# Performance work log

Hardware: AMD Instinct MI355X
Metric: run time of the kernel (lower is better)

## Reference

```python
import jax, jax.numpy as jnp
import numpy as np

D_MODEL = 1024
NUM_HEADS = 16
HEAD_DIM = D_MODEL // NUM_HEADS
THETA = 10000.0
B, T = 2, 2048


def setup_inputs() -> dict:
    key = jax.random.key(0)
    k1, k2, k3 = jax.random.split(key, 3)
    x = jax.random.normal(k1, (B, T, D_MODEL), dtype=jnp.float32)
    W_qkv = jax.random.normal(k2, (3 * D_MODEL, D_MODEL), dtype=jnp.float32) * 0.02
    W_o = jax.random.normal(k3, (D_MODEL, D_MODEL), dtype=jnp.float32) * 0.02
    return {"x": x, "W_qkv": W_qkv, "W_o": W_o}


def _rope(x, cos, sin):
    # x: [B, h, T, d]; rotate interleaved even/odd pairs
    x_even = x[..., 0::2]
    x_odd = x[..., 1::2]
    out_even = x_even * cos - x_odd * sin
    out_odd = x_even * sin + x_odd * cos
    out = jnp.stack([out_even, out_odd], axis=-1)  # [B,h,T,d/2,2]
    return out.reshape(x.shape)


def reference(x, W_qkv, W_o):
    b, t, dm = x.shape
    # fused QKV projection (bias-free Linear: x @ W.T)
    qkv = jnp.einsum('btd,ed->bte', x, W_qkv)                # [B,T,3*D]
    qkv = qkv.reshape(b, t, 3, NUM_HEADS, HEAD_DIM)
    qkv = jnp.transpose(qkv, (2, 0, 3, 1, 4))                # [3,B,h,T,d]
    q, k, v = qkv[0], qkv[1], qkv[2]

    # RoPE with token_positions = arange(T)
    pos = jnp.arange(t, dtype=jnp.float32)                   # [T]
    inv_freq = THETA ** (-jnp.arange(0, HEAD_DIM, 2, dtype=jnp.float32) / HEAD_DIM)
    ang = pos[:, None] * inv_freq[None, :]                   # [T, d/2]
    cos = jnp.cos(ang)[None, None, :, :]
    sin = jnp.sin(ang)[None, None, :, :]
    q = _rope(q, cos, sin)
    k = _rope(k, cos, sin)

    # causal scaled dot-product attention
    scale = 1.0 / jnp.sqrt(jnp.asarray(HEAD_DIM, dtype=x.dtype))
    scores = jnp.einsum('bhqd,bhkd->bhqk', q, k) * scale     # [B,h,T,T]
    causal = jnp.tril(jnp.ones((t, t), dtype=bool))
    scores = jnp.where(causal[None, None, :, :], scores, -jnp.inf)
    attn = jax.nn.softmax(scores, axis=-1)
    out = jnp.einsum('bhqk,bhkd->bhqd', attn, v)             # [B,h,T,d]
    out = jnp.transpose(out, (0, 2, 1, 3)).reshape(b, t, dm) # [B,T,D]
    return jnp.einsum('btd,ed->bte', out, W_o)
```

## Files before the change

kernel.cpp:

```cpp
#include <hip/hip_runtime.h>
#include <hip/hip_bf16.h>
#include <cstdint>

#define NHEADS 16
#define HDIM 64
#define BB 2
#define TSEQ 2048
#define DM 1024
#define MROWS (BB*TSEQ)

typedef unsigned short u16;
typedef unsigned int u32;
typedef __bf16 bf16x8 __attribute__((ext_vector_type(8)));
typedef float f32x4 __attribute__((ext_vector_type(4)));

#define AS1C(p) ((const __attribute__((address_space(1))) u32*)(p))
#define AS3(p)  ((__attribute__((address_space(3))) u32*)(p))

static __device__ __forceinline__ u16 f2bf(float f) {
  return __builtin_bit_cast(u16, __float2bfloat16(f));
}
static __device__ __forceinline__ float bf2f(u16 u) {
  return __bfloat162float(__builtin_bit_cast(__hip_bfloat16, u));
}
static __device__ __forceinline__ u32 pack2bf(float a, float b) {
  const u32 ua = __builtin_bit_cast(u32, a) + 0x8000u;
  const u32 ub = __builtin_bit_cast(u32, b) + 0x8000u;
  return (ua >> 16) | (ub & 0xFFFF0000u);
}
static __device__ __forceinline__ f32x4 mfma16x16(bf16x8 a, bf16x8 b, f32x4 c) {
  return __builtin_amdgcn_mfma_f32_16x16x32_bf16(a, b, c, 0, 0, 0);
}

#define N4_X   (MROWS * DM / 4)
#define N4_WQ  (3 * DM * DM / 4)
#define N4_WO  (DM * DM / 4)
__global__ __launch_bounds__(256) void cast_all(const float* __restrict__ x,
                                                const float* __restrict__ wq,
                                                const float* __restrict__ wo,
                                                u16* __restrict__ xb,
                                                u16* __restrict__ wqb,
                                                u16* __restrict__ wob) {
  int i = blockIdx.x * 256 + threadIdx.x;
  const int stride = gridDim.x * 256;
  for (; i < N4_X + N4_WQ + N4_WO; i += stride) {
    const float4* src; u16* dst; int j;
    if (i < N4_X)            { src = (const float4*)x;  dst = xb;  j = i; }
    else if (i < N4_X + N4_WQ) { src = (const float4*)wq; dst = wqb; j = i - N4_X; }
    else                     { src = (const float4*)wo; dst = wob; j = i - N4_X - N4_WQ; }
    float4 v = src[j];
    ushort4 o;
    o.x = f2bf(v.x); o.y = f2bf(v.y); o.z = f2bf(v.z); o.w = f2bf(v.w);
    ((ushort4*)dst)[j] = o;
  }
}

template<int WRITE_BF16>
__global__ __launch_bounds__(256, 2) void gemm_bt(const u16* __restrict__ A,
                                                  const u16* __restrict__ Bm,
                                                  float* __restrict__ Cf,
                                                  u16* __restrict__ Cb,
                                                  int M, int N, int K) {
  __shared__ u16 lA[2][128 * 32];
  __shared__ u16 lB[2][128 * 32];
  const int tid = threadIdx.x;
  const int w = tid >> 6, l = tid & 63;
  const int wr = w >> 1, wc = w & 1;
  int bid = blockIdx.y * gridDim.x + blockIdx.x;
  const int cpx = (gridDim.x * gridDim.y) >> 3;
  bid = (bid & 7) * cpx + (bid >> 3);
  const int bx = bid % gridDim.x, by = bid / gridDim.x;
  const int brow = by * 128, bcol = bx * 128;
  const int lr = l & 15, lg = l >> 4;

  const int srow = l >> 2;
  const int scol = (((l & 3) ^ (srow & 3)) * 8);

  auto stage = [&](int buf, int k0) {
#pragma unroll
    for (int is = 0; is < 2; ++is) {
      const int chunk = w * 2 + is;
      const int row = chunk * 16 + srow;
      __builtin_amdgcn_global_load_lds(AS1C(A + (size_t)(brow + row) * K + k0 + scol),
                                       AS3((char*)lA[buf] + chunk * 1024), 16, 0, 0);
      __builtin_amdgcn_global_load_lds(AS1C(Bm + (size_t)(bcol + row) * K + k0 + scol),
                                       AS3((char*)lB[buf] + chunk * 1024), 16, 0, 0);
    }
  };

  f32x4 acc[4][4] = {};
  const int nk = K >> 5;
  stage(0, 0);
  for (int kk = 0; kk < nk; ++kk) {
    const int cur = kk & 1;
    __syncthreads();
    if (kk + 1 < nk) stage(cur ^ 1, (kk + 1) << 5);
    bf16x8 af[4], bfr[4];
#pragma unroll
    for (int m = 0; m < 4; ++m) {
      const int row = wr * 64 + m * 16 + lr;
      const int sl = lg ^ (row & 3);
      af[m] = *(const bf16x8*)(&lA[cur][row * 32 + sl * 8]);
    }
#pragma unroll
    for (int n = 0; n < 4; ++n) {
      const int row = wc * 64 + n * 16 + lr;
      const int sl = lg ^ (row & 3);
      bfr[n] = *(const bf16x8*)(&lB[cur][row * 32 + sl * 8]);
    }
#pragma unroll
    for (int m = 0; m < 4; ++m)
#pragma unroll
      for (int n = 0; n < 4; ++n)
        acc[m][n] = mfma16x16(af[m], bfr[n], acc[m][n]);
  }
#pragma unroll
  for (int m = 0; m < 4; ++m)
#pragma unroll
    for (int n = 0; n < 4; ++n)
#pragma unroll
      for (int r = 0; r < 4; ++r) {
        const int row = brow + wr * 64 + m * 16 + lg * 4 + r;
        const int col = bcol + wc * 64 + n * 16 + lr;
        if constexpr (WRITE_BF16)
          Cb[(size_t)row * N + col] = f2bf(acc[m][n][r]);
        else
          Cf[(size_t)row * N + col] = acc[m][n][r];
      }
}

__global__ __launch_bounds__(256) void rope_reshape(const u16* __restrict__ qkvb,
                                                    u16* __restrict__ qb,
                                                    u16* __restrict__ kb,
                                                    u16* __restrict__ vbT) {
  const int bh = blockIdx.y;
  const int b = bh >> 4, h = bh & 15;
  const int t0 = blockIdx.x * 64;
  const int tid = threadIdx.x;
  const float C = -0.4152410118609203f;
  const float QS = 0.125f * 1.44269504088896341f;

  for (int idx = tid; idx < 64 * 32; idx += 256) {
    const int tl = idx >> 5, p = idx & 31;
    const int t = t0 + tl;
    const size_t base = ((size_t)(b * TSEQ + t)) * 3072 + h * 64 + 2 * p;
    const float qe = bf2f(qkvb[base]), qo = bf2f(qkvb[base + 1]);
    const float ke = bf2f(qkvb[base + 1024]), ko = bf2f(qkvb[base + 1025]);
    const float inv = exp2f((float)p * C);
    const float ang = (float)t * inv;
    float sn, cs;
    sincosf(ang, &sn, &cs);
    const size_t ob = ((size_t)bh * TSEQ + t) * 64 + 2 * p;
    qb[ob]     = f2bf((qe * cs - qo * sn) * QS);
    qb[ob + 1] = f2bf((qe * sn + qo * cs) * QS);
    kb[ob]     = f2bf(ke * cs - ko * sn);
    kb[ob + 1] = f2bf(ke * sn + ko * cs);
  }

  __shared__ u16 lT[64][65];
  for (int idx = tid; idx < 64 * 64; idx += 256) {
    const int tl = idx >> 6, d = idx & 63;
    lT[tl][d] = qkvb[((size_t)(b * TSEQ + t0 + tl)) * 3072 + 2048 + h * 64 + d];
  }
  __syncthreads();
  for (int idx = tid; idx < 64 * 64; idx += 256) {
    const int d = idx >> 6, tl = idx & 63;
    vbT[((size_t)bh * 64 + d) * TSEQ + t0 + tl] = lT[tl][d];
  }
}

__global__ __launch_bounds__(256, 4) void attn_fwd(const u16* __restrict__ qb,
                                                   const u16* __restrict__ kb,
                                                   const u16* __restrict__ vbT,
                                                   u16* __restrict__ ob) {
  __shared__ u16 lK[2][2][32 * 64];
  __shared__ u16 lV[2][2][64 * 32];
  __shared__ u16 lP[4][16 * 40];
  const int hw = blockIdx.x;
  const int logical = (hw & 7) * 64 + (hw >> 3);
  const int bh = logical >> 4;
  const int pair = logical & 15;
  const int b = bh >> 4, h = bh & 15;
  const int tid = threadIdx.x;
  const int w = tid >> 6, l = tid & 63;
  const int g = w >> 1, wq = w & 1;
  const int lr = l & 15, lg = l >> 4;
  const int kscol = ((l & 7) ^ (l >> 3)) * 8;
  const int vscol = ((l & 3) ^ ((l >> 2) & 3)) * 8;
  const u16* Kb = kb + (size_t)bh * TSEQ * 64;
  const u16* Vb = vbT + (size_t)bh * 64 * TSEQ;
  u16* lPw = lP[w];

  auto stage = [&](int buf, int kt) {
#pragma unroll
    for (int is = 0; is < 2; ++is) {
      const int chunk = wq * 2 + is;
      const int krow = chunk * 8 + (l >> 3);
      __builtin_amdgcn_global_load_lds(AS1C(Kb + (size_t)(kt * 32 + krow) * 64 + kscol),
                                       AS3((char*)lK[g][buf] + chunk * 1024), 16, 0, 0);
      const int vrow = chunk * 16 + (l >> 2);
      __builtin_amdgcn_global_load_lds(AS1C(Vb + (size_t)vrow * TSEQ + kt * 32 + vscol),
                                       AS3((char*)lV[g][buf] + chunk * 1024), 16, 0, 0);
    }
  };

  for (int half = 0; half < 2; ++half) {
    const int qt = half ? (31 - pair) : pair;
    const int q0 = qt * 64;
    const int ts = 2 * qt + wq;
    const int qa0 = q0 + wq * 32 + lr;

    bf16x8 qf[2][2];
    {
      const u16* qp = qb + ((size_t)bh * TSEQ + q0 + wq * 32 + lr) * 64 + lg * 8;
      qf[0][0] = *(const bf16x8*)qp;
      qf[0][1] = *(const bf16x8*)(qp + 32);
      qp += 16 * 64;
      qf[1][0] = *(const bf16x8*)qp;
      qf[1][1] = *(const bf16x8*)(qp + 32);
    }

    f32x4 o0[4] = {}, o1[4] = {};
    float ls0 = 0.f, ls1 = 0.f;

    __syncthreads();
    stage(0, g);
    for (int it = 0; it <= qt; ++it) {
      const int cur = it & 1;
      __syncthreads();
      if (it < qt) stage(cur ^ 1, 2 * (it + 1) + g);
      const int kt = 2 * it + g;
      if (kt <= ts) {
        const u16* Kc = lK[g][cur];
        const u16* Vc = lV[g][cur];

        bf16x8 kf[2][2];
#pragma unroll
        for (int n = 0; n < 2; ++n) {
          const int row = n * 16 + lr;
#pragma unroll
          for (int ks = 0; ks < 2; ++ks)
            kf[n][ks] = *(const bf16x8*)(&Kc[row * 64 + (((ks * 4 + lg) ^ (row & 7)) * 8)]);
        }
        f32x4 s0[2] = {}, s1[2] = {};
        __builtin_amdgcn_s_setprio(1);
#pragma unroll
        for (int n = 0; n < 2; ++n)
#pragma unroll
          for (int ks = 0; ks < 2; ++ks) {
            s0[n] = mfma16x16(kf[n][ks], qf[0][ks], s0[n]);
            s1[n] = mfma16x16(kf[n][ks], qf[1][ks], s1[n]);
          }
        __builtin_amdgcn_s_setprio(0);

        const bool diag = (kt == ts);
        const int kvb = kt * 32;

#pragma unroll
        for (int n = 0; n < 2; ++n) {
          float pv[4];
#pragma unroll
          for (int r = 0; r < 4; ++r) {
            float p = __builtin_amdgcn_exp2f(s0[n][r]);
            if (diag && (kvb + n * 16 + lg * 4 + r > qa0)) p = 0.f;
            pv[r] = p;
            ls0 += p;
          }
          uint2 pk; pk.x = pack2bf(pv[0], pv[1]); pk.y = pack2bf(pv[2], pv[3]);
          *(uint2*)(&lPw[lr * 40 + n * 16 + lg * 4]) = pk;
        }
        bf16x8 pf0 = *(const bf16x8*)(&lPw[lr * 40 + lg * 8]);

#pragma unroll
        for (int n = 0; n < 2; ++n) {
          float pv[4];
#pragma unroll
          for (int r = 0; r < 4; ++r) {
            float p = __builtin_amdgcn_exp2f(s1[n][r]);
            if (diag && (kvb + n * 16 + lg * 4 + r > qa0 + 16)) p = 0.f;
            pv[r] = p;
            ls1 += p;
          }
          uint2 pk; pk.x = pack2bf(pv[0], pv[1]); pk.y = pack2bf(pv[2], pv[3]);
          *(uint2*)(&lPw[lr * 40 + n * 16 + lg * 4]) = pk;
        }
        bf16x8 pf1 = *(const bf16x8*)(&lPw[lr * 40 + lg * 8]);

        __builtin_amdgcn_s_setprio(1);
#pragma unroll
        for (int n = 0; n < 4; ++n) {
          const int row = n * 16 + lr;
          bf16x8 vf = *(const bf16x8*)(&Vc[row * 32 + ((lg ^ (row & 3)) * 8)]);
          o0[n] = mfma16x16(vf, pf0, o0[n]);
          o1[n] = mfma16x16(vf, pf1, o1[n]);
        }
        __builtin_amdgcn_s_setprio(0);
      }
    }

    ls0 += __shfl_xor(ls0, 16); ls0 += __shfl_xor(ls0, 32);
    ls1 += __shfl_xor(ls1, 16); ls1 += __shfl_xor(ls1, 32);

    __syncthreads();
    float* mO = (float*)&lK[0][0][0];
    float* mL = (float*)&lV[0][0][0];
    if (g == 1) {
#pragma unroll
      for (int qs = 0; qs < 2; ++qs)
#pragma unroll
        for (int n = 0; n < 4; ++n)
#pragma unroll
          for (int r = 0; r < 4; ++r) {
            const int d = n * 16 + lg * 4 + r;
            mO[((wq * 2 + qs) * 64 + d) * 16 + lr] = (qs ? o1[n][r] : o0[n][r]);
          }
      if (lg == 0) {
        mL[(wq * 2 + 0) * 16 + lr] = ls0;
        mL[(wq * 2 + 1) * 16 + lr] = ls1;
      }
    }
    __syncthreads();
    if (g == 0) {
      const float rl0 = 1.f / (ls0 + mL[(wq * 2 + 0) * 16 + lr]);
      const float rl1 = 1.f / (ls1 + mL[(wq * 2 + 1) * 16 + lr]);
#pragma unroll
      for (int qs = 0; qs < 2; ++qs) {
        const int q = q0 + wq * 32 + qs * 16 + lr;
        const float rl = qs ? rl1 : rl0;
#pragma unroll
        for (int n = 0; n < 4; ++n) {
          ushort4 ov;
#pragma unroll
          for (int r = 0; r < 4; ++r) {
            const int d = n * 16 + lg * 4 + r;
            const float o = (qs ? o1[n][r] : o0[n][r]) + mO[((wq * 2 + qs) * 64 + d) * 16 + lr];
            ((u16*)&ov)[r] = f2bf(o * rl);
          }
          *(ushort4*)(&ob[(size_t)(b * TSEQ + q) * DM + h * 64 + n * 16 + lg * 4]) = ov;
        }
      }
    }
  }
}

extern "C" void kernel_launch(void* const* d_in, const int* in_sizes, int n_in,
                              void* d_out, int out_size, void* d_ws, size_t ws_size,
                              hipStream_t stream) {
  const float* x    = (const float*)d_in[0];
  const float* Wqkv = (const float*)d_in[1];
  const float* Wo   = (const float*)d_in[2];
  float* out = (float*)d_out;

  char* ws = (char*)d_ws;
  u16* xb    = (u16*)ws; ws += (size_t)MROWS * DM * 2;
  u16* wqkvb = (u16*)ws; ws += (size_t)3 * DM * DM * 2;
  u16* wob   = (u16*)ws; ws += (size_t)DM * DM * 2;
  u16* qkvb  = (u16*)ws; ws += (size_t)MROWS * 3 * DM * 2;
  u16* qb    = (u16*)ws; ws += (size_t)BB * NHEADS * TSEQ * HDIM * 2;
  u16* kb    = (u16*)ws; ws += (size_t)BB * NHEADS * TSEQ * HDIM * 2;
  u16* vbT   = (u16*)ws; ws += (size_t)BB * NHEADS * TSEQ * HDIM * 2;
  u16* ob    = (u16*)ws; ws += (size_t)MROWS * DM * 2;

  cast_all<<<2048, 256, 0, stream>>>(x, Wqkv, Wo, xb, wqkvb, wob);

  gemm_bt<1><<<dim3(3 * DM / 128, MROWS / 128), 256, 0, stream>>>(
      xb, wqkvb, nullptr, qkvb, MROWS, 3 * DM, DM);

  rope_reshape<<<dim3(TSEQ / 64, BB * NHEADS), 256, 0, stream>>>(qkvb, qb, kb, vbT);

  attn_fwd<<<512, 256, 0, stream>>>(qb, kb, vbT, ob);

  gemm_bt<0><<<dim3(DM / 128, MROWS / 128), 256, 0, stream>>>(
      ob, wob, out, nullptr, MROWS, DM, DM);
}
```

Before: 121.3 us.

## Split attention KV range into four partial blocks with a separate merge kernel

Each attention block now handles a 128-row query tile and one quarter of its causal KV range, giving 1024 blocks with all four waves working on separate query rows and sharing a single K/V stage. Partial unnormalized outputs (bf16) and row sums go to scratch that reuses the dead cast/QKV workspace. A new merge kernel sums them and normalizes. RoPE is also vectorized with 16-byte loads and stores and uses hardware sin/cos on a range-reduced angle. The intent is better load balance and occupancy, paid for with extra scratch traffic, an additional launch, and bf16 rounding of the partial sums.

```diff
diff --git a/kernel.cpp b/kernel.cpp
--- a/kernel.cpp
+++ b/kernel.cpp
@@ -139,22 +139,32 @@
   const int tid = threadIdx.x;
   const float C = -0.4152410118609203f;
   const float QS = 0.125f * 1.44269504088896341f;
-
-  for (int idx = tid; idx < 64 * 32; idx += 256) {
-    const int tl = idx >> 5, p = idx & 31;
+  const float R2PI = 0.15915494309189535f;
+
+  for (int idx = tid; idx < 64 * 8; idx += 256) {
+    const int tl = idx >> 3, grp = idx & 7;
     const int t = t0 + tl;
-    const size_t base = ((size_t)(b * TSEQ + t)) * 3072 + h * 64 + 2 * p;
-    const float qe = bf2f(qkvb[base]), qo = bf2f(qkvb[base + 1]);
-    const float ke = bf2f(qkvb[base + 1024]), ko = bf2f(qkvb[base + 1025]);
-    const float inv = exp2f((float)p * C);
-    const float ang = (float)t * inv;
-    float sn, cs;
-    sincosf(ang, &sn, &cs);
-    const size_t ob = ((size_t)bh * TSEQ + t) * 64 + 2 * p;
-    qb[ob]     = f2bf((qe * cs - qo * sn) * QS);
-    qb[ob + 1] = f2bf((qe * sn + qo * cs) * QS);
-    kb[ob]     = f2bf(ke * cs - ko * sn);
-    kb[ob + 1] = f2bf(ke * sn + ko * cs);
+    const size_t base = ((size_t)(b * TSEQ + t)) * 3072 + h * 64 + grp * 8;
+    u16 qv[8], kv8[8], qo[8], ko[8];
+    *(uint4*)qv  = *(const uint4*)(qkvb + base);
+    *(uint4*)kv8 = *(const uint4*)(qkvb + base + 1024);
+#pragma unroll
+    for (int j = 0; j < 4; ++j) {
+      const int p = grp * 4 + j;
+      const float inv = exp2f((float)p * C);
+      const float rev = __builtin_amdgcn_fractf((float)t * inv * R2PI);
+      const float sn = __builtin_amdgcn_sinf(rev);
+      const float cs = __builtin_amdgcn_cosf(rev);
+      const float qe = bf2f(qv[2 * j]), qoo = bf2f(qv[2 * j + 1]);
+      const float ke = bf2f(kv8[2 * j]), koo = bf2f(kv8[2 * j + 1]);
+      qo[2 * j]     = f2bf((qe * cs - qoo * sn) * QS);
+      qo[2 * j + 1] = f2bf((qe * sn + qoo * cs) * QS);
+      ko[2 * j]     = f2bf(ke * cs - koo * sn);
+      ko[2 * j + 1] = f2bf(ke * sn + koo * cs);
+    }
+    const size_t obase = ((size_t)bh * TSEQ + t) * 64 + grp * 8;
+    *(uint4*)(qb + obase) = *(uint4*)qo;
+    *(uint4*)(kb + obase) = *(uint4*)ko;
   }
 
   __shared__ u16 lT[64][65];
@@ -172,47 +182,46 @@
 __global__ __launch_bounds__(256, 4) void attn_fwd(const u16* __restrict__ qb,
                                                    const u16* __restrict__ kb,
                                                    const u16* __restrict__ vbT,
-                                                   u16* __restrict__ ob) {
-  __shared__ u16 lK[2][2][32 * 64];
-  __shared__ u16 lV[2][2][64 * 32];
+                                                   u16* __restrict__ pO,
+                                                   float* __restrict__ pL) {
+  __shared__ u16 lK[2][32 * 64];
+  __shared__ u16 lV[2][64 * 32];
   __shared__ u16 lP[4][16 * 40];
   const int hw = blockIdx.x;
-  const int logical = (hw & 7) * 64 + (hw >> 3);
-  const int bh = logical >> 4;
-  const int pair = logical & 15;
-  const int b = bh >> 4, h = bh & 15;
+  const int logical = (hw & 7) * 128 + (hw >> 3);
+  const int bh = logical >> 5;
+  const int s = logical & 31;
+  const int jA = s & 15, qA = s >> 4;
   const int tid = threadIdx.x;
   const int w = tid >> 6, l = tid & 63;
-  const int g = w >> 1, wq = w & 1;
   const int lr = l & 15, lg = l >> 4;
   const int kscol = ((l & 7) ^ (l >> 3)) * 8;
-  const int vscol = ((l & 3) ^ ((l >> 2) & 3)) * 8;
+  const int vscol = ((l & 3) ^ ((l >> 3) & 3)) * 8;
   const u16* Kb = kb + (size_t)bh * TSEQ * 64;
   const u16* Vb = vbT + (size_t)bh * 64 * TSEQ;
   u16* lPw = lP[w];
 
   auto stage = [&](int buf, int kt) {
-#pragma unroll
-    for (int is = 0; is < 2; ++is) {
-      const int chunk = wq * 2 + is;
-      const int krow = chunk * 8 + (l >> 3);
-      __builtin_amdgcn_global_load_lds(AS1C(Kb + (size_t)(kt * 32 + krow) * 64 + kscol),
-                                       AS3((char*)lK[g][buf] + chunk * 1024), 16, 0, 0);
-      const int vrow = chunk * 16 + (l >> 2);
-      __builtin_amdgcn_global_load_lds(AS1C(Vb + (size_t)vrow * TSEQ + kt * 32 + vscol),
-                                       AS3((char*)lV[g][buf] + chunk * 1024), 16, 0, 0);
-    }
+    const int krow = w * 8 + (l >> 3);
+    __builtin_amdgcn_global_load_lds(AS1C(Kb + (size_t)(kt * 32 + krow) * 64 + kscol),
+                                     AS3((char*)lK[buf] + w * 1024), 16, 0, 0);
+    const int vrow = w * 16 + (l >> 2);
+    __builtin_amdgcn_global_load_lds(AS1C(Vb + (size_t)vrow * TSEQ + kt * 32 + vscol),
+                                     AS3((char*)lV[buf] + w * 1024), 16, 0, 0);
   };
 
-  for (int half = 0; half < 2; ++half) {
-    const int qt = half ? (31 - pair) : pair;
-    const int q0 = qt * 64;
-    const int ts = 2 * qt + wq;
-    const int qa0 = q0 + wq * 32 + lr;
+  for (int task = 0; task < 2; ++task) {
+    const int j  = task ? (15 - jA) : jA;
+    const int qq = task ? (3 - qA) : qA;
+    const int nt = j + 1;
+    const int kt0 = qq * nt;
+    const int q0 = j * 128;
+    const int ktd = 4 * j + w;
+    const int qa0 = q0 + w * 32 + lr;
 
     bf16x8 qf[2][2];
     {
-      const u16* qp = qb + ((size_t)bh * TSEQ + q0 + wq * 32 + lr) * 64 + lg * 8;
+      const u16* qp = qb + ((size_t)bh * TSEQ + q0 + w * 32 + lr) * 64 + lg * 8;
       qf[0][0] = *(const bf16x8*)qp;
       qf[0][1] = *(const bf16x8*)(qp + 32);
       qp += 16 * 64;
@@ -224,15 +233,15 @@
     float ls0 = 0.f, ls1 = 0.f;
 
     __syncthreads();
-    stage(0, g);
-    for (int it = 0; it <= qt; ++it) {
+    stage(0, kt0);
+    for (int it = 0; it < nt; ++it) {
       const int cur = it & 1;
       __syncthreads();
-      if (it < qt) stage(cur ^ 1, 2 * (it + 1) + g);
-      const int kt = 2 * it + g;
-      if (kt <= ts) {
-        const u16* Kc = lK[g][cur];
-        const u16* Vc = lV[g][cur];
+      if (it + 1 < nt) stage(cur ^ 1, kt0 + it + 1);
+      const int kt = kt0 + it;
+      if (kt <= ktd) {
+        const u16* Kc = lK[cur];
+        const u16* Vc = lV[cur];
 
         bf16x8 kf[2][2];
 #pragma unroll
@@ -253,7 +262,7 @@
           }
         __builtin_amdgcn_s_setprio(0);
 
-        const bool diag = (kt == ts);
+        const bool diag = (kt == ktd);
         const int kvb = kt * 32;
 
 #pragma unroll
@@ -290,7 +299,7 @@
 #pragma unroll
         for (int n = 0; n < 4; ++n) {
           const int row = n * 16 + lr;
-          bf16x8 vf = *(const bf16x8*)(&Vc[row * 32 + ((lg ^ (row & 3)) * 8)]);
+          bf16x8 vf = *(const bf16x8*)(&Vc[row * 32 + ((lg ^ ((row >> 1) & 3)) * 8)]);
           o0[n] = mfma16x16(vf, pf0, o0[n]);
           o1[n] = mfma16x16(vf, pf1, o1[n]);
         }
@@ -301,46 +310,59 @@
     ls0 += __shfl_xor(ls0, 16); ls0 += __shfl_xor(ls0, 32);
     ls1 += __shfl_xor(ls1, 16); ls1 += __shfl_xor(ls1, 32);
 
-    __syncthreads();
-    float* mO = (float*)&lK[0][0][0];
-    float* mL = (float*)&lV[0][0][0];
-    if (g == 1) {
-#pragma unroll
-      for (int qs = 0; qs < 2; ++qs)
-#pragma unroll
-        for (int n = 0; n < 4; ++n)
-#pragma unroll
-          for (int r = 0; r < 4; ++r) {
-            const int d = n * 16 + lg * 4 + r;
-            mO[((wq * 2 + qs) * 64 + d) * 16 + lr] = (qs ? o1[n][r] : o0[n][r]);
-          }
-      if (lg == 0) {
-        mL[(wq * 2 + 0) * 16 + lr] = ls0;
-        mL[(wq * 2 + 1) * 16 + lr] = ls1;
+    const size_t pbase = ((size_t)(qq * 32 + bh)) * TSEQ;
+#pragma unroll
+    for (int qs = 0; qs < 2; ++qs) {
+      const int row = q0 + w * 32 + qs * 16 + lr;
+#pragma unroll
+      for (int n = 0; n < 4; ++n) {
+        uint2 ov;
+        if (qs == 0) { ov.x = pack2bf(o0[n][0], o0[n][1]); ov.y = pack2bf(o0[n][2], o0[n][3]); }
+        else         { ov.x = pack2bf(o1[n][0], o1[n][1]); ov.y = pack2bf(o1[n][2], o1[n][3]); }
+        *(uint2*)(&pO[(pbase + row) * 64 + n * 16 + lg * 4]) = ov;
       }
     }
-    __syncthreads();
-    if (g == 0) {
-      const float rl0 = 1.f / (ls0 + mL[(wq * 2 + 0) * 16 + lr]);
-      const float rl1 = 1.f / (ls1 + mL[(wq * 2 + 1) * 16 + lr]);
-#pragma unroll
-      for (int qs = 0; qs < 2; ++qs) {
-        const int q = q0 + wq * 32 + qs * 16 + lr;
-        const float rl = qs ? rl1 : rl0;
-#pragma unroll
-        for (int n = 0; n < 4; ++n) {
-          ushort4 ov;
-#pragma unroll
-          for (int r = 0; r < 4; ++r) {
-            const int d = n * 16 + lg * 4 + r;
-            const float o = (qs ? o1[n][r] : o0[n][r]) + mO[((wq * 2 + qs) * 64 + d) * 16 + lr];
-            ((u16*)&ov)[r] = f2bf(o * rl);
-          }
-          *(ushort4*)(&ob[(size_t)(b * TSEQ + q) * DM + h * 64 + n * 16 + lg * 4]) = ov;
-        }
-      }
-    }
-  }
+    if (lg == 0) {
+      pL[pbase + q0 + w * 32 + lr] = ls0;
+      pL[pbase + q0 + w * 32 + 16 + lr] = ls1;
+    }
+  }
+}
+
+__global__ __launch_bounds__(256) void attn_merge(const u16* __restrict__ pO,
+                                                  const float* __restrict__ pL,
+                                                  u16* __restrict__ ob) {
+  const int hw = blockIdx.x;
+  const int logical = (hw & 7) * 64 + (hw >> 3);
+  const int bh = logical >> 4;
+  const int rseg = logical & 15;
+  const int b = bh >> 4, h = bh & 15;
+  const int tid = threadIdx.x;
+  const int row = rseg * 128 + (tid >> 1);
+  const int dh = (tid & 1) * 32;
+
+  float acc[32] = {};
+  float lsum = 0.f;
+#pragma unroll
+  for (int q = 0; q < 4; ++q) {
+    const size_t pbase = ((size_t)(q * 32 + bh)) * TSEQ + row;
+    lsum += pL[pbase];
+#pragma unroll
+    for (int k = 0; k < 4; ++k) {
+      uint4 v = *(const uint4*)(pO + pbase * 64 + dh + k * 8);
+      const u16* pv = (const u16*)&v;
+#pragma unroll
+      for (int e = 0; e < 8; ++e) acc[k * 8 + e] += bf2f(pv[e]);
+    }
+  }
+  const float rl = 1.f / lsum;
+  u16 outv[32];
+#pragma unroll
+  for (int e = 0; e < 32; ++e) outv[e] = f2bf(acc[e] * rl);
+  u16* dst = ob + ((size_t)(b * TSEQ) + row) * DM + h * 64 + dh;
+#pragma unroll
+  for (int k = 0; k < 4; ++k)
+    *(uint4*)(dst + k * 8) = ((uint4*)outv)[k];
 }
 
 extern "C" void kernel_launch(void* const* d_in, const int* in_sizes, int n_in,
@@ -352,14 +374,19 @@
   float* out = (float*)d_out;
 
   char* ws = (char*)d_ws;
-  u16* xb    = (u16*)ws; ws += (size_t)MROWS * DM * 2;
-  u16* wqkvb = (u16*)ws; ws += (size_t)3 * DM * DM * 2;
-  u16* wob   = (u16*)ws; ws += (size_t)DM * DM * 2;
-  u16* qkvb  = (u16*)ws; ws += (size_t)MROWS * 3 * DM * 2;
-  u16* qb    = (u16*)ws; ws += (size_t)BB * NHEADS * TSEQ * HDIM * 2;
-  u16* kb    = (u16*)ws; ws += (size_t)BB * NHEADS * TSEQ * HDIM * 2;
-  u16* vbT   = (u16*)ws; ws += (size_t)BB * NHEADS * TSEQ * HDIM * 2;
-  u16* ob    = (u16*)ws; ws += (size_t)MROWS * DM * 2;
+  char* regA = ws;
+  u16* xb    = (u16*)regA;
+  u16* wqkvb = (u16*)(regA + (size_t)MROWS * DM * 2);
+  u16* qkvb  = (u16*)(regA + (size_t)MROWS * DM * 2 + (size_t)3 * DM * DM * 2);
+  ws += (size_t)MROWS * DM * 2 + (size_t)3 * DM * DM * 2 + (size_t)MROWS * 3 * DM * 2;
+  u16* pO = (u16*)regA;
+  float* pL = (float*)(regA + (size_t)4 * 32 * TSEQ * 64 * 2);
+
+  u16* wob = (u16*)ws; ws += (size_t)DM * DM * 2;
+  u16* qb  = (u16*)ws; ws += (size_t)BB * NHEADS * TSEQ * HDIM * 2;
+  u16* kb  = (u16*)ws; ws += (size_t)BB * NHEADS * TSEQ * HDIM * 2;
+  u16* vbT = (u16*)ws; ws += (size_t)BB * NHEADS * TSEQ * HDIM * 2;
+  u16* ob  = (u16*)ws; ws += (size_t)MROWS * DM * 2;
 
   cast_all<<<2048, 256, 0, stream>>>(x, Wqkv, Wo, xb, wqkvb, wob);
 
@@ -368,7 +395,9 @@
 
   rope_reshape<<<dim3(TSEQ / 64, BB * NHEADS), 256, 0, stream>>>(qkvb, qb, kb, vbT);
 
-  attn_fwd<<<512, 256, 0, stream>>>(qb, kb, vbT, ob);
+  attn_fwd<<<1024, 256, 0, stream>>>(qb, kb, vbT, pO, pL);
+
+  attn_merge<<<512, 256, 0, stream>>>(pO, pL, ob);
 
   gemm_bt<0><<<dim3(DM / 128, MROWS / 128), 256, 0, stream>>>(
       ob, wob, out, nullptr, MROWS, DM, DM);
```

After: 124.3 us. 2.5% more time.
